# Performance work log

Hardware: AMD Instinct MI355X
Metric: run time of the kernel (lower is better)

## Reference

```python
import jax, jax.numpy as jnp
import numpy as np

BS, F, C, H, W = 2, 8, 64, 128, 128
HEADS = 4

def build_edges(bs, f):
    rows, cols, ec = [], [], 0
    for b in range(bs):
        s = b * (2 * f + 2)
        v = list(range(s, s + f)); d = list(range(s + f, s + 2 * f))
        t = s + 2 * f; g = t + 1
        for grp in (v, d, v + d, v + d, v + d + [t], [t], [g]):
            rows += grp; cols += [ec] * len(grp); ec += 1
    return np.asarray(rows, np.int32), np.asarray(cols, np.int32), ec

ROW, COL, NUM_EDGES = build_edges(BS, F)

def conv2d_s2(x, w, b):  # Conv2d k3 s2 p1 + ReLU
    y = jax.lax.conv_general_dilated(x, w, (2, 2), [(1, 1), (1, 1)],
        dimension_numbers=('NCHW', 'OIHW', 'NCHW'))
    return jax.nn.relu(y + b[None, :, None, None])

def conv_t2(x, w, b):  # ConvTranspose2d k3 s2 p1 op1 + ReLU; w: (in,out,3,3)
    wt = jnp.flip(w, (2, 3)).transpose(1, 0, 2, 3)
    y = jax.lax.conv_general_dilated(x, wt, (1, 1), [(1, 2), (1, 2)],
        lhs_dilation=(2, 2), dimension_numbers=('NCHW', 'OIHW', 'NCHW'))
    return jax.nn.relu(y + b[None, :, None, None])

def layer_norm(x, eps=1e-5):  # affine params are default ones/zeros
    mu = x.mean(-1, keepdims=True)
    var = ((x - mu) ** 2).mean(-1, keepdims=True)
    return (x - mu) / jnp.sqrt(var + eps)

def group_norm(x, groups=32, eps=1e-5):
    n, c = x.shape
    xg = x.reshape(n, groups, c // groups)
    mu = xg.mean(-1, keepdims=True)
    var = ((xg - mu) ** 2).mean(-1, keepdims=True)
    return ((xg - mu) / jnp.sqrt(var + eps)).reshape(n, c)

def se_layer(x, w1, w2):  # squeeze over node dim 0
    y = jax.nn.sigmoid(jax.nn.relu(x.mean(0) @ w1.T) @ w2.T)
    return x * y

def hypergraph_conv(x, lin_w, att, edge_w, edge_attr, out_ch):
    # PyG HypergraphConv, use_attention=True, attention_mode='node', heads=4,
    # concat=False, bias=False, eval mode (dropout inactive)
    n = x.shape[0]
    xl = (x @ lin_w.T).reshape(n, HEADS, out_ch)
    ea = (edge_attr @ lin_w.T).reshape(-1, HEADS, out_ch)
    a = (jnp.concatenate([xl[ROW], ea[COL]], axis=-1) * att).sum(-1)  # (E, heads)
    a = jax.nn.leaky_relu(a, 0.2)
    a = jnp.exp(a - jax.ops.segment_max(a, COL, num_segments=NUM_EDGES)[COL])
    a = a / (jax.ops.segment_sum(a, COL, num_segments=NUM_EDGES)[COL] + 1e-16)
    D = jax.ops.segment_sum(edge_w[COL], ROW, num_segments=n)
    D = jnp.where(D > 0, 1.0 / D, 0.0)
    B = jax.ops.segment_sum(jnp.ones(ROW.shape[0], x.dtype), COL, num_segments=NUM_EDGES)
    B = jnp.where(B > 0, 1.0 / B, 0.0)
    e = jax.ops.segment_sum(B[COL][:, None, None] * a[:, :, None] * xl[ROW], COL, num_segments=NUM_EDGES)
    o = jax.ops.segment_sum(D[ROW][:, None, None] * a[:, :, None] * e[COL], ROW, num_segments=n)
    return o.mean(1)  # concat=False -> head mean

def setup_inputs() -> dict:
    key = jax.random.key(0)
    ks = jax.random.split(key, 32)
    def n(k, shape, s=1.0):
        return jax.random.normal(k, shape, jnp.float32) * s
    def u(k, shape):
        return jax.random.uniform(k, shape, jnp.float32)
    return {
        'vision_feat': n(ks[0], (BS, F, C, H, W)), 'vision_pos': n(ks[1], (BS, F, C, H, W), 0.1),
        'motion_feat': n(ks[2], (BS, F, C, H, W)), 'motion_pos': n(ks[3], (BS, F, C, H, W), 0.1),
        'text_feat': n(ks[4], (BS, C, 16)), 'text_pos': n(ks[5], (BS, C, 16), 0.1),
        'cv1_w': n(ks[6], (2 * C, C, 3, 3), 0.04), 'cv1_b': n(ks[7], (2 * C,), 0.01),
        'cv2_w': n(ks[8], (4 * C, 2 * C, 3, 3), 0.03), 'cv2_b': n(ks[9], (4 * C,), 0.01),
        'dc1_w': n(ks[10], (2 * C, C, 3, 3), 0.04), 'dc1_b': n(ks[11], (2 * C,), 0.01),
        'dc2_w': n(ks[12], (4 * C, 2 * C, 3, 3), 0.03), 'dc2_b': n(ks[13], (4 * C,), 0.01),
        'tc1_w': n(ks[14], (4 * C, 2 * C, 3, 3), 0.03), 'tc1_b': n(ks[15], (2 * C,), 0.01),
        'tc2_w': n(ks[16], (2 * C, C, 3, 3), 0.04), 'tc2_b': n(ks[17], (C,), 0.01),
        'lin1_w': n(ks[18], (HEADS * 8 * C, 4 * C), 0.06), 'att1': n(ks[19], (1, HEADS, 16 * C), 0.05),
        'lin2_w': n(ks[20], (HEADS * 4 * C, 8 * C), 0.04), 'att2': n(ks[21], (1, HEADS, 8 * C), 0.05),
        'ew1': u(ks[22], (2 * F * BS + 2,)), 'ew2': u(ks[23], (2 * F * BS + 2,)),
        'ea1': u(ks[24], (2 * F * BS + 2, 4 * C)), 'ea2': u(ks[25], (2 * F * BS + 2, 8 * C)),
        'se1_w1': n(ks[26], (8 * C // 16, 8 * C), 0.06), 'se1_w2': n(ks[27], (8 * C, 8 * C // 16), 0.15),
        'se2_w1': n(ks[28], (4 * C // 16, 4 * C), 0.08), 'se2_w2': n(ks[29], (4 * C, 4 * C // 16), 0.2),
    }

def reference(vision_feat, vision_pos, motion_feat, motion_pos, text_feat, text_pos,
              cv1_w, cv1_b, cv2_w, cv2_b, dc1_w, dc1_b, dc2_w, dc2_b,
              tc1_w, tc1_b, tc2_w, tc2_b, lin1_w, att1, lin2_w, att2,
              ew1, ew2, ea1, ea2, se1_w1, se1_w2, se2_w1, se2_w2):
    bs, f, c, h, w = vision_feat.shape
    # text_pool: AdaptiveMaxPool1d(4) on L=16 -> exact windows of 4; view(bs,-1)
    tn = (text_feat + text_pos).reshape(bs, c, 4, 4).max(-1).reshape(bs, 4 * c)
    v0 = (vision_feat + vision_pos).reshape(bs * f, c, h, w)
    v1 = conv2d_s2(v0, cv1_w, cv1_b)          # (bs*f, 2c, h/2, w/2)
    v2 = conv2d_s2(v1, cv2_w, cv2_b)          # (bs*f, 4c, h/4, w/4)
    vn = layer_norm(v2.max((2, 3)))           # AdaptiveMaxPool2d(1) + LayerNorm
    d0 = (motion_feat + motion_pos).reshape(bs * f, c, h, w)
    dn = layer_norm(conv2d_s2(conv2d_s2(d0, dc1_w, dc1_b), dc2_w, dc2_b).max((2, 3)))
    vb = vn.reshape(bs, f, 4 * c); db = dn.reshape(bs, f, 4 * c)
    obs = tn + (vb + db).mean(1)              # observer = mean(text+v+d) over frames
    x = jnp.concatenate([vb, db, tn[:, None], obs[:, None]], axis=1).reshape(bs * (2 * f + 2), 4 * c)
    x = se_layer(group_norm(jax.nn.relu(hypergraph_conv(x, lin1_w, att1, ew1, ea1, 8 * c))), se1_w1, se1_w2)
    x = se_layer(group_norm(jax.nn.relu(hypergraph_conv(x, lin2_w, att2, ew2, ea2, 4 * c))), se2_w1, se2_w2)
    xb = x.reshape(bs, 2 * f + 2, 4 * c)
    # obs_pool: AdaptiveMaxPool1d(c) on L=4c -> windows of 4
    observers = (tn + xb[:, -1]).reshape(bs, c, 4).max(-1)
    vg = xb[:, :f].reshape(bs * f, 4 * c)
    # bilinear upsample of 1x1 == broadcast; transconv doubles size so the
    # subsequent F.interpolate calls to (h/2,w/2) and (h,w) are identities
    vr = v2 + vg[:, :, None, None]
    vr = v1 + conv_t2(vr, tc1_w, tc1_b)
    vr = v0 + conv_t2(vr, tc2_w, tc2_b)
    return vr, observers
```

## Files before the change

kernel.cpp:

```cpp
#include <hip/hip_runtime.h>
#include <hip/hip_bf16.h>
#include <cstddef>
#include <cstdint>

#define DEV_INLINE __device__ __forceinline__
#define AS1 __attribute__((address_space(1)))
#define AS3 __attribute__((address_space(3)))

typedef __attribute__((ext_vector_type(8))) short short8;
typedef __attribute__((ext_vector_type(4))) float f32x4;
typedef __attribute__((ext_vector_type(2))) float f32x2;
typedef __attribute__((ext_vector_type(4))) unsigned short us4;

DEV_INLINE unsigned short f2bf(float f) {
  uint32_t u = __builtin_bit_cast(uint32_t, f);
  uint32_t r = (u + 0x7fffu + ((u >> 16) & 1u)) >> 16;
  return (unsigned short)r;
}
DEV_INLINE float bf2f(unsigned short u) {
  return __builtin_bit_cast(float, (uint32_t)u << 16);
}

DEV_INLINE void gl_lds16(const float* g, float* l) {
  __builtin_amdgcn_global_load_lds((AS1 void*)const_cast<float*>(g),
                                   (AS3 void*)l, 16, 0, 0);
}

__device__ __constant__ int c_cs[15] = {0,8,16,32,48,65,66,67,75,83,99,115,132,133,134};
__device__ __constant__ int c_row[134] = {
  0,1,2,3,4,5,6,7,
  8,9,10,11,12,13,14,15,
  0,1,2,3,4,5,6,7,8,9,10,11,12,13,14,15,
  0,1,2,3,4,5,6,7,8,9,10,11,12,13,14,15,
  0,1,2,3,4,5,6,7,8,9,10,11,12,13,14,15,16,
  16,
  17,
  18,19,20,21,22,23,24,25,
  26,27,28,29,30,31,32,33,
  18,19,20,21,22,23,24,25,26,27,28,29,30,31,32,33,
  18,19,20,21,22,23,24,25,26,27,28,29,30,31,32,33,
  18,19,20,21,22,23,24,25,26,27,28,29,30,31,32,33,34,
  34,
  35
};
__device__ __constant__ int c_col[134] = {
  0,0,0,0,0,0,0,0,
  1,1,1,1,1,1,1,1,
  2,2,2,2,2,2,2,2,2,2,2,2,2,2,2,2,
  3,3,3,3,3,3,3,3,3,3,3,3,3,3,3,3,
  4,4,4,4,4,4,4,4,4,4,4,4,4,4,4,4,4,
  5,
  6,
  7,7,7,7,7,7,7,7,
  8,8,8,8,8,8,8,8,
  9,9,9,9,9,9,9,9,9,9,9,9,9,9,9,9,
  10,10,10,10,10,10,10,10,10,10,10,10,10,10,10,10,
  11,11,11,11,11,11,11,11,11,11,11,11,11,11,11,11,11,
  12,
  13
};

__global__ __launch_bounds__(512) void k_prep(const float* __restrict__ a,
                                              const float* __restrict__ b,
                                              unsigned short* __restrict__ o) {
  __shared__ float sbuf[32 * 260];
  int bid = blockIdx.x;
  int y = bid & 127, n = bid >> 7;
  int t = threadIdx.x;
  int w = t >> 6, lane = t & 63;
  int cio = lane >> 5;
  int xg4 = (lane & 31) * 4;
  const size_t base = ((size_t)n * 64) * 16384 + (size_t)y * 128;
#pragma unroll
  for (int k = 0; k < 4; ++k) {
    int c = w * 4 + k;
    gl_lds16(a + base + (size_t)(2 * c + cio) * 16384 + xg4, &sbuf[c * 260]);
  }
  __syncthreads();
  auto rd = [&](int ci, int x) {
    return sbuf[(ci >> 1) * 260 + (ci & 1) * 128 + x];
  };
  float av[2][8];
#pragma unroll
  for (int it = 0; it < 2; ++it) {
    int i = t + it * 512;
    int x = i >> 3, cq = i & 7;
#pragma unroll
    for (int j = 0; j < 8; ++j) av[it][j] = rd(cq * 8 + j, x);
  }
  __syncthreads();
#pragma unroll
  for (int k = 0; k < 4; ++k) {
    int c = w * 4 + k;
    gl_lds16(b + base + (size_t)(2 * c + cio) * 16384 + xg4, &sbuf[c * 260]);
  }
  __syncthreads();
  unsigned int* op = (unsigned int*)(o + (((size_t)n * 128 + y) * 128) * 64);
#pragma unroll
  for (int it = 0; it < 2; ++it) {
    int i = t + it * 512;
    int x = i >> 3, cq = i & 7;
    uint4 v;
    unsigned int vv[4];
#pragma unroll
    for (int jj = 0; jj < 4; ++jj) {
      unsigned int lo = f2bf(av[it][2 * jj]     + rd(cq * 8 + 2 * jj, x));
      unsigned int hi = f2bf(av[it][2 * jj + 1] + rd(cq * 8 + 2 * jj + 1, x));
      vv[jj] = lo | (hi << 16);
    }
    v.x = vv[0]; v.y = vv[1]; v.z = vv[2]; v.w = vv[3];
    *reinterpret_cast<uint4*>(op + x * 32 + cq * 4) = v;
  }
}

__global__ void k_wtrans_all(const float* __restrict__ cv1w, const float* __restrict__ dc1w,
                             const float* __restrict__ cv2w, const float* __restrict__ dc2w,
                             const float* __restrict__ tc1w, const float* __restrict__ tc2w,
                             unsigned short* __restrict__ wtb) {
  int idx = blockIdx.x * 256 + threadIdx.x;
  const float* src; int off, lci, lco; bool tra;
  if (idx < 73728)        { src = cv1w; off = 0;       lci = 6; lco = 7; tra = false; }
  else if (idx < 147456)  { src = dc1w; off = 73728;   lci = 6; lco = 7; tra = false; }
  else if (idx < 442368)  { src = cv2w; off = 147456;  lci = 7; lco = 8; tra = false; }
  else if (idx < 737280)  { src = dc2w; off = 442368;  lci = 7; lco = 8; tra = false; }
  else if (idx < 1032192) { src = tc1w; off = 737280;  lci = 8; lco = 7; tra = true;  }
  else if (idx < 1105920) { src = tc2w; off = 1032192; lci = 7; lco = 6; tra = true;  }
  else return;
  int l = idx - off;
  int ci = l & ((1 << lci) - 1);
  int r = l >> lci;
  int co = r & ((1 << lco) - 1);
  int tap = r >> lco;
  size_t si = tra ? (((size_t)ci << lco) + co) * 9 + tap
                  : (((size_t)co << lci) + ci) * 9 + tap;
  wtb[idx] = f2bf(src[si]);
}

template<int CI, int CO, int HO, int WO, int ROUT, bool SPLIT_IN>
__global__ __launch_bounds__(512, 3) void k_conv_mfma_b(
    const unsigned short* __restrict__ in0, const unsigned short* __restrict__ in1,
    const unsigned short* __restrict__ wT0, const unsigned short* __restrict__ wT1,
    const float* __restrict__ b0, const float* __restrict__ b1,
    unsigned short* __restrict__ outn) {
  constexpr int HIN = HO * 2, WIN = WO * 2;
  constexpr int XHP = WO + 2;
  constexpr int R = 2 * ROUT + 1;
  constexpr int NPOS = R * 2 * XHP;
  static_assert(NPOS <= 512, "one staging position per thread");
  constexpr int NCS = CI / 32;
  constexpr int CB = CO / 128;
  constexpr int OB = HO / ROUT;
  __shared__ short8 sIn[4 * NPOS];
  int bid = blockIdx.x;
  int cb = bid % CB; bid /= CB;
  int oyb = bid % OB; int n = bid / OB;
  int br = n >> 4;
  const unsigned short* in = SPLIT_IN ? (br ? in1 : in0) : in0;
  const unsigned short* wT = br ? wT1 : wT0;
  const float* bias = br ? b1 : b0;
  int ni = SPLIT_IN ? (n & 15) : n;
  int tid = threadIdx.x;
  int wid = tid >> 6, lane = tid & 63;
  int wm = wid >> 1, wn = wid & 1;
  int llo = lane & 15, lhi = lane >> 4;
  f32x4 acc[2][2] = {};
  const int iy0 = oyb * (2 * ROUT) - 1;
  bool sact = tid < NPOS;
  int sx = 0, siy = 0; bool sok = false;
  if (sact) {
    int xh = tid % XHP; int q2 = tid / XHP;
    int par = q2 & 1, l = q2 >> 1;
    sx = 2 * xh + par - 1;
    siy = iy0 + l;
    sok = (sx >= 0 && sx < WIN && siy >= 0 && siy < HIN);
    if (!sok) { sx = 0; siy = 0; }
  }
  short8 rv[4];
  auto loadr = [&](int cs) {
    if (sact) {
      const unsigned short* gp = in + ((((size_t)ni * HIN + siy) * WIN + sx) * CI + cs * 32);
#pragma unroll
      for (int c = 0; c < 4; ++c) {
        short8 v = {};
        if (sok) v = *reinterpret_cast<const short8*>(gp + c * 8);
        rv[c] = v;
      }
    }
  };
  auto writes = [&]() {
    if (sact) {
#pragma unroll
      for (int c = 0; c < 4; ++c) sIn[c * NPOS + tid] = rv[c];
    }
  };
  loadr(0);
  for (int cs = 0; cs < NCS; ++cs) {
    writes();
    __syncthreads();
    if (cs + 1 < NCS) loadr(cs + 1);
    short8 afr9[9][2];
#pragma unroll
    for (int tap = 0; tap < 9; ++tap)
#pragma unroll
      for (int m = 0; m < 2; ++m) {
        int co = cb * 128 + wm * 32 + m * 16 + llo;
        afr9[tap][m] = *reinterpret_cast<const short8*>(wT + (((size_t)tap * CO + co) * CI + cs * 32 + lhi * 8));
      }
#pragma unroll
    for (int tap = 0; tap < 9; ++tap) {
      const int ky = tap / 3, kx = tap % 3;
      short8 bfr[2];
#pragma unroll
      for (int n2 = 0; n2 < 2; ++n2) {
        int pix = wn * 32 + n2 * 16 + llo;
        int oyl = (ROUT == 2) ? (pix >> 5) : 0;
        int ox = pix - oyl * WO;
        int lrow = 2 * oyl + ky;
        int pos = (lrow * 2 + (kx & 1)) * XHP + ox + (kx >> 1);
        bfr[n2] = sIn[lhi * NPOS + pos];
      }
#pragma unroll
      for (int m = 0; m < 2; ++m)
#pragma unroll
        for (int n2 = 0; n2 < 2; ++n2)
          acc[m][n2] = __builtin_amdgcn_mfma_f32_16x16x32_bf16(afr9[tap][m], bfr[n2], acc[m][n2], 0, 0, 0);
    }
    __syncthreads();
  }
#pragma unroll
  for (int m = 0; m < 2; ++m) {
    int co0 = cb * 128 + wm * 32 + m * 16 + lhi * 4;
    f32x4 bv = *reinterpret_cast<const f32x4*>(bias + co0);
#pragma unroll
    for (int n2 = 0; n2 < 2; ++n2) {
      int pix = wn * 32 + n2 * 16 + llo;
      int oyl = (ROUT == 2) ? (pix >> 5) : 0;
      int ox = pix - oyl * WO;
      int oy = oyb * ROUT + oyl;
      us4 pk;
      pk[0] = f2bf(fmaxf(acc[m][n2][0] + bv[0], 0.f));
      pk[1] = f2bf(fmaxf(acc[m][n2][1] + bv[1], 0.f));
      pk[2] = f2bf(fmaxf(acc[m][n2][2] + bv[2], 0.f));
      pk[3] = f2bf(fmaxf(acc[m][n2][3] + bv[3], 0.f));
      *reinterpret_cast<us4*>(outn + ((((size_t)n * HO + oy) * WO + ox) * CO + co0)) = pk;
    }
  }
}

template<int CI, int CO, int Hi, int Wi, int QR, bool OBF, bool GADD>
__global__ __launch_bounds__(256, 3) void k_deconv_mfma(
    const unsigned short* __restrict__ in,
    const unsigned short* __restrict__ wT,
    const float* __restrict__ bias,
    const unsigned short* __restrict__ resn,
    const float* __restrict__ gsrc,
    unsigned short* __restrict__ outn,
    float* __restrict__ outc) {
  constexpr int QC = 64 / QR;
  constexpr int WP = Wi + 1;
  constexpr int NPOS = (QR + 1) * WP;
  static_assert(NPOS <= 256, "one staging position per thread");
  constexpr int NCS = CI / 32;
  constexpr int CB = CO / 64;
  constexpr int OB = Hi / QR;
  constexpr int Ho = Hi * 2, Wo = Wi * 2;
  __shared__ short8 sIn[4 * NPOS];
  int bid = blockIdx.x;
  int cb = bid % CB; bid /= CB;
  int oyb = bid % OB; int n = bid / OB;
  int tid = threadIdx.x;
  int wid = tid >> 6, lane = tid & 63;
  int wm = wid >> 1, wn = wid & 1;
  int llo = lane & 15, lhi = lane >> 4;
  int qy0 = oyb * QR;
  const float* g = nullptr;
  if constexpr (GADD) g = gsrc + ((size_t)((n >> 3) * 18 + (n & 7))) * 256;
  f32x4 acc[4][2][2] = {};
  constexpr int tap_p[9] = {3,2,3,1,0,1,3,2,3};
  constexpr int tap_b[9] = {3,2,2,1,0,0,1,0,0};
  bool sact = tid < NPOS;
  int sx = 0, siy = 0; bool sok = false;
  if (sact) {
    sx = tid % WP;
    siy = qy0 + tid / WP;
    sok = (sx < Wi && siy < Hi);
    if (!sok) { sx = 0; siy = 0; }
  }
  short8 rv[4];
  auto loadr = [&](int cs) {
    if (sact) {
      const unsigned short* gp = in + (((size_t)(n * Hi + siy) * Wi + sx) * CI + cs * 32);
#pragma unroll
      for (int c = 0; c < 4; ++c) {
        short8 v = {};
        if (sok) {
          v = *reinterpret_cast<const short8*>(gp + c * 8);
          if constexpr (GADD) {
#pragma unroll
            for (int j = 0; j < 8; ++j) {
              float fv = bf2f((unsigned short)v[j]) + g[cs * 32 + c * 8 + j];
              v[j] = (short)f2bf(fv);
            }
          }
        }
        rv[c] = v;
      }
    }
  };
  auto writes = [&]() {
    if (sact) {
#pragma unroll
      for (int c = 0; c < 4; ++c) sIn[c * NPOS + tid] = rv[c];
    }
  };
  loadr(0);
  for (int cs = 0; cs < NCS; ++cs) {
    writes();
    __syncthreads();
    if (cs + 1 < NCS) loadr(cs + 1);
    short8 bfr[2][4];
#pragma unroll
    for (int n2 = 0; n2 < 2; ++n2) {
      int pix = wn * 32 + n2 * 16 + llo;
      int qyl = pix / QC, qx = pix % QC;
#pragma unroll
      for (int bs = 0; bs < 4; ++bs) {
        int pos = (qyl + (bs >> 1)) * WP + qx + (bs & 1);
        bfr[n2][bs] = sIn[lhi * NPOS + pos];
      }
    }
#pragma unroll
    for (int m = 0; m < 2; ++m) {
      short8 afr9[9];
#pragma unroll
      for (int tap = 0; tap < 9; ++tap) {
        int co = cb * 64 + wm * 32 + m * 16 + llo;
        afr9[tap] = *reinterpret_cast<const short8*>(wT + (((size_t)tap * CO + co) * CI + cs * 32 + lhi * 8));
      }
#pragma unroll
      for (int tap = 0; tap < 9; ++tap)
#pragma unroll
        for (int n2 = 0; n2 < 2; ++n2)
          acc[tap_p[tap]][m][n2] = __builtin_amdgcn_mfma_f32_16x16x32_bf16(
              afr9[tap], bfr[n2][tap_b[tap]], acc[tap_p[tap]][m][n2], 0, 0, 0);
    }
    __syncthreads();
  }
#pragma unroll
  for (int m = 0; m < 2; ++m) {
    int co0 = cb * 64 + wm * 32 + m * 16 + lhi * 4;
    f32x4 bv = *reinterpret_cast<const f32x4*>(bias + co0);
#pragma unroll
    for (int n2 = 0; n2 < 2; ++n2) {
      int pix = wn * 32 + n2 * 16 + llo;
      int qyl = pix / QC, qx = pix % QC;
      int qy = qy0 + qyl;
      if constexpr (OBF) {
#pragma unroll
        for (int p = 0; p < 4; ++p) {
          int oy = 2 * qy + (p >> 1);
          int ox = 2 * qx + (p & 1);
          size_t ad = ((size_t)(n * Ho + oy) * Wo + ox) * CO + co0;
          us4 r = *reinterpret_cast<const us4*>(resn + ad);
          us4 pk;
#pragma unroll
          for (int c = 0; c < 4; ++c)
            pk[c] = f2bf(bf2f(r[c]) + fmaxf(acc[p][m][n2][c] + bv[c], 0.f));
          *reinterpret_cast<us4*>(outn + ad) = pk;
        }
      } else {
        int qx2 = 2 * qx;
#pragma unroll
        for (int dy = 0; dy < 2; ++dy) {
          int oy = 2 * qy + dy;
          size_t rb = ((size_t)(n * Ho + oy) * Wo + qx2) * CO + co0;
          us4 r0 = *reinterpret_cast<const us4*>(resn + rb);
          us4 r1 = *reinterpret_cast<const us4*>(resn + rb + CO);
#pragma unroll
          for (int c = 0; c < 4; ++c) {
            f32x2 st;
            st[0] = bf2f(r0[c]) + fmaxf(acc[dy * 2][m][n2][c] + bv[c], 0.f);
            st[1] = bf2f(r1[c]) + fmaxf(acc[dy * 2 + 1][m][n2][c] + bv[c], 0.f);
            __builtin_nontemporal_store(st,
                reinterpret_cast<f32x2*>(outc + ((size_t)(n * CO + co0 + c) * Ho + oy) * Wo + qx2));
          }
        }
      }
    }
  }
}

__global__ __launch_bounds__(256) void k_max_part(const unsigned short* __restrict__ x,
                                                  float* __restrict__ pmax) {
  int n = blockIdx.x >> 3, pg = blockIdx.x & 7;
  int t = threadIdx.x;
  int c8 = t & 31;
  int ps = t >> 5;
  const unsigned short* base = x + (size_t)n * 262144 + (size_t)pg * 32768 + (size_t)c8 * 8;
  float m[8];
#pragma unroll
  for (int j = 0; j < 8; ++j) m[j] = -1e30f;
  for (int p = ps * 16; p < ps * 16 + 16; ++p) {
    short8 v = *reinterpret_cast<const short8*>(base + (size_t)p * 256);
#pragma unroll
    for (int j = 0; j < 8; ++j) m[j] = fmaxf(m[j], bf2f((unsigned short)v[j]));
  }
  __shared__ float sred[8][264];
#pragma unroll
  for (int j = 0; j < 8; ++j) sred[ps][c8 * 8 + j] = m[j];
  __syncthreads();
  float mm = sred[0][t];
#pragma unroll
  for (int g = 1; g < 8; ++g) mm = fmaxf(mm, sred[g][t]);
  pmax[((size_t)n * 8 + pg) * 256 + t] = mm;
}

__global__ __launch_bounds__(256) void k_ln(const float* __restrict__ pmax,
                                            float* __restrict__ out) {
  int n = blockIdx.x, ch = threadIdx.x;
  float m = -1e30f;
#pragma unroll
  for (int g = 0; g < 8; ++g)
    m = fmaxf(m, pmax[((size_t)n * 8 + g) * 256 + ch]);
  __shared__ float r1[256], r2[256];
  r1[ch] = m; __syncthreads();
  for (int s = 128; s > 0; s >>= 1) { if (ch < s) r1[ch] += r1[ch + s]; __syncthreads(); }
  float mu = r1[0] * (1.f / 256.f);
  float d = m - mu;
  r2[ch] = d * d; __syncthreads();
  for (int s = 128; s > 0; s >>= 1) { if (ch < s) r2[ch] += r2[ch + s]; __syncthreads(); }
  out[(size_t)n * 256 + ch] = d * rsqrtf(r2[0] * (1.f / 256.f) + 1e-5f);
}

__global__ void k_build_x(const float* __restrict__ tf, const float* __restrict__ tp,
                          const float* __restrict__ nb,
                          float* __restrict__ tn, float* __restrict__ x0) {
  int b = blockIdx.x, ch = threadIdx.x;
  int c4 = ch >> 2, j = ch & 3;
  const float* p = tf + ((size_t)b * 64 + c4) * 16 + j * 4;
  const float* q = tp + ((size_t)b * 64 + c4) * 16 + j * 4;
  float tv = p[0] + q[0];
  tv = fmaxf(tv, p[1] + q[1]);
  tv = fmaxf(tv, p[2] + q[2]);
  tv = fmaxf(tv, p[3] + q[3]);
  tn[(size_t)b * 256 + ch] = tv;
  const float* dn = nb;
  const float* vn = nb + 16 * 256;
  float s = 0.f;
  for (int f = 0; f < 8; ++f) {
    float vv = vn[((size_t)b * 8 + f) * 256 + ch];
    float dd = dn[((size_t)b * 8 + f) * 256 + ch];
    s += vv + dd;
    x0[((size_t)b * 18 + f) * 256 + ch] = vv;
    x0[((size_t)b * 18 + 8 + f) * 256 + ch] = dd;
  }
  x0[((size_t)b * 18 + 16) * 256 + ch] = tv;
  x0[((size_t)b * 18 + 17) * 256 + ch] = tv + s * (1.f / 8.f);
}

__global__ __launch_bounds__(256) void k_gnn_lin(
    const float* __restrict__ x, const float* __restrict__ ea,
    const float* __restrict__ w, float* __restrict__ y, int K, int M) {
  int chunks = M >> 8;
  int r = blockIdx.x / chunks;
  int ob = (blockIdx.x % chunks) * 256 + threadIdx.x;
  const float* src = (r < 36) ? (x + (size_t)r * K) : (ea + (size_t)(r - 36) * K);
  __shared__ __align__(16) float sxr[512];
  for (int k = threadIdx.x; k < K; k += 256) sxr[k] = src[k];
  __syncthreads();
  const float4* w4 = reinterpret_cast<const float4*>(w + (size_t)ob * K);
  const float4* x4 = reinterpret_cast<const float4*>(sxr);
  float acc = 0.f;
  int k4 = K >> 2;
  for (int k = 0; k < k4; ++k) {
    float4 a = x4[k], b = w4[k];
    acc += a.x * b.x + a.y * b.y + a.z * b.z + a.w * b.w;
  }
  y[(size_t)r * M + ob] = acc;
}

template<int OC>
__global__ __launch_bounds__(256) void k_gnn_attsm(
    const float* __restrict__ y, const float* __restrict__ att,
    float* __restrict__ attw) {
  int t = threadIdx.x;
  __shared__ float sx_s[144], seb_s[60];
  __shared__ float a_s[536];
  if (t < 200) {
    int r = t >> 2, h = t & 3;
    const float4* row = reinterpret_cast<const float4*>(y + ((size_t)r * 4 + h) * OC);
    const float4* ar = reinterpret_cast<const float4*>(att + (size_t)h * 2 * OC + (r < 36 ? 0 : OC));
    float s = 0.f;
#pragma unroll 4
    for (int k = 0; k < OC / 4; ++k) {
      float4 a = row[k], b = ar[k];
      s += a.x * b.x + a.y * b.y + a.z * b.z + a.w * b.w;
    }
    if (r < 36) sx_s[r * 4 + h] = s; else seb_s[(r - 36) * 4 + h] = s;
  }
  __syncthreads();
  for (int idx = t; idx < 536; idx += 256) {
    int i = idx >> 2, h = idx & 3;
    float v = sx_s[c_row[i] * 4 + h] + seb_s[c_col[i] * 4 + h];
    a_s[idx] = (v > 0.f) ? v : 0.2f * v;
  }
  __syncthreads();
  if (t < 56) {
    int c = t >> 2, h = t & 3;
    int st = c_cs[c], en = c_cs[c + 1];
    float m = -1e30f;
    for (int i = st; i < en; ++i) m = fmaxf(m, a_s[i * 4 + h]);
    float s = 0.f;
    for (int i = st; i < en; ++i) { float e = __expf(a_s[i * 4 + h] - m); a_s[i * 4 + h] = e; s += e; }
    float inv = 1.f / (s + 1e-16f);
    for (int i = st; i < en; ++i) a_s[i * 4 + h] *= inv;
  }
  __syncthreads();
  for (int idx = t; idx < 536; idx += 256) attw[idx] = a_s[idx];
}

template<int OC>
__global__ __launch_bounds__(256) void k_edge_agg(
    const float* __restrict__ y, const float* __restrict__ attw,
    float* __restrict__ eb) {
  int idx = blockIdx.x * 256 + threadIdx.x;
  if (idx >= 14 * 4 * OC) return;
  int ch = idx % OC;
  int h = (idx / OC) & 3;
  int c = idx / (4 * OC);
  int st = c_cs[c], en = c_cs[c + 1];
  float s = 0.f;
  for (int i = st; i < en; ++i)
    s += attw[i * 4 + h] * y[(size_t)c_row[i] * (4 * OC) + h * OC + ch];
  eb[idx] = s * (1.f / (float)(en - st));
}

template<int OC>
__global__ __launch_bounds__(256) void k_node_agg(
    const float* __restrict__ attw, const float* __restrict__ eb,
    const float* __restrict__ ew, float* __restrict__ ho) {
  int idx = blockIdx.x * 256 + threadIdx.x;
  if (idx >= 36 * OC) return;
  int ch = idx % OC;
  int node = idx / OC;
  int b = node / 18, ln = node % 18;
  int ncols, cols[4], gis[4];
  if (ln < 16) {
    ncols = 4;
    cols[0] = b * 7 + (ln < 8 ? 0 : 1); gis[0] = b * 67 + ln;
    cols[1] = b * 7 + 2; gis[1] = b * 67 + 16 + ln;
    cols[2] = b * 7 + 3; gis[2] = b * 67 + 32 + ln;
    cols[3] = b * 7 + 4; gis[3] = b * 67 + 48 + ln;
  } else if (ln == 16) {
    ncols = 2;
    cols[0] = b * 7 + 4; gis[0] = b * 67 + 64;
    cols[1] = b * 7 + 5; gis[1] = b * 67 + 65;
    cols[2] = cols[3] = 0; gis[2] = gis[3] = 0;
  } else {
    ncols = 1;
    cols[0] = b * 7 + 6; gis[0] = b * 67 + 66;
    cols[1] = cols[2] = cols[3] = 0; gis[1] = gis[2] = gis[3] = 0;
  }
  float dsum = 0.f;
#pragma unroll
  for (int k = 0; k < 4; ++k) if (k < ncols) dsum += ew[cols[k]];
  float D = dsum > 0.f ? 1.f / dsum : 0.f;
  float s = 0.f;
#pragma unroll
  for (int k = 0; k < 4; ++k) {
    if (k < ncols) {
#pragma unroll
      for (int h = 0; h < 4; ++h)
        s += attw[gis[k] * 4 + h] * eb[((size_t)cols[k] * 4 + h) * OC + ch];
    }
  }
  ho[idx] = fmaxf(0.25f * D * s, 0.f);
}

template<int C, int Cr>
__global__ __launch_bounds__(512) void k_gn_se(
    const float* __restrict__ hin, const float* __restrict__ w1,
    const float* __restrict__ w2, float* __restrict__ x) {
  int t = threadIdx.x;
  constexpr int gs = C >> 5;
  for (int idx = t; idx < 36 * 32; idx += 512) {
    int node = idx >> 5, g = idx & 31;
    const float* p = hin + (size_t)node * C + g * gs;
    float s = 0.f, s2 = 0.f;
#pragma unroll
    for (int k = 0; k < gs; ++k) { float v = p[k]; s += v; s2 += v * v; }
    float mu = s * (1.f / gs);
    float var = s2 * (1.f / gs) - mu * mu;
    float inv = rsqrtf(fmaxf(var, 0.f) + 1e-5f);
    float* q = x + (size_t)node * C + g * gs;
#pragma unroll
    for (int k = 0; k < gs; ++k) q[k] = (p[k] - mu) * inv;
  }
  __threadfence_block();
  __syncthreads();
  __shared__ float smean[C];
  __shared__ float spart[Cr][17];
  __shared__ float shid[Cr];
  __shared__ float sscale[C];
  if (t < C) {
    float s = 0.f;
    for (int nn = 0; nn < 36; ++nn) s += x[(size_t)nn * C + t];
    smean[t] = s * (1.f / 36.f);
  }
  __syncthreads();
  if (t < Cr * 16) {
    int hid = t >> 4, sub = t & 15;
    constexpr int CH = C / 16;
    float s = 0.f;
#pragma unroll
    for (int k = 0; k < CH; ++k)
      s += w1[(size_t)hid * C + sub * CH + k] * smean[sub * CH + k];
    spart[hid][sub] = s;
  }
  __syncthreads();
  if (t < Cr) {
    float s = 0.f;
#pragma unroll
    for (int k = 0; k < 16; ++k) s += spart[t][k];
    shid[t] = fmaxf(s, 0.f);
  }
  __syncthreads();
  if (t < C) {
    float s = 0.f;
#pragma unroll
    for (int k = 0; k < Cr; ++k) s += w2[(size_t)t * Cr + k] * shid[k];
    sscale[t] = 1.f / (1.f + __expf(-s));
  }
  __syncthreads();
  for (int idx = t; idx < 36 * C; idx += 512) x[idx] *= sscale[idx % C];
}

__global__ void k_obs(const float* __restrict__ tn, const float* __restrict__ x2,
                      float* __restrict__ out) {
  int t = threadIdx.x;
  if (t >= 128) return;
  int b = t >> 6, ch = t & 63;
  const float* a = tn + (size_t)b * 256 + ch * 4;
  const float* c = x2 + ((size_t)b * 18 + 17) * 256 + ch * 4;
  float m = a[0] + c[0];
  m = fmaxf(m, a[1] + c[1]);
  m = fmaxf(m, a[2] + c[2]);
  m = fmaxf(m, a[3] + c[3]);
  out[b * 64 + ch] = m;
}

extern "C" void kernel_launch(void* const* d_in, const int* in_sizes, int n_in,
                              void* d_out, int out_size, void* d_ws, size_t ws_size,
                              hipStream_t stream) {
  (void)in_sizes; (void)n_in; (void)out_size; (void)ws_size;
  const float* vf    = (const float*)d_in[0];
  const float* vp    = (const float*)d_in[1];
  const float* mf    = (const float*)d_in[2];
  const float* mp    = (const float*)d_in[3];
  const float* tf    = (const float*)d_in[4];
  const float* tp    = (const float*)d_in[5];
  const float* cv1w  = (const float*)d_in[6];
  const float* cv1b  = (const float*)d_in[7];
  const float* cv2w  = (const float*)d_in[8];
  const float* cv2b  = (const float*)d_in[9];
  const float* dc1w  = (const float*)d_in[10];
  const float* dc1b  = (const float*)d_in[11];
  const float* dc2w  = (const float*)d_in[12];
  const float* dc2b  = (const float*)d_in[13];
  const float* tc1w  = (const float*)d_in[14];
  const float* tc1b  = (const float*)d_in[15];
  const float* tc2w  = (const float*)d_in[16];
  const float* tc2b  = (const float*)d_in[17];
  const float* lin1w = (const float*)d_in[18];
  const float* att1  = (const float*)d_in[19];
  const float* lin2w = (const float*)d_in[20];
  const float* att2  = (const float*)d_in[21];
  const float* ew1   = (const float*)d_in[22];
  const float* ew2   = (const float*)d_in[23];
  const float* ea1   = (const float*)d_in[24];
  const float* ea2   = (const float*)d_in[25];
  const float* se1w1 = (const float*)d_in[26];
  const float* se1w2 = (const float*)d_in[27];
  const float* se2w1 = (const float*)d_in[28];
  const float* se2w2 = (const float*)d_in[29];

  float* ws  = (float*)d_ws;
  float* out = (float*)d_out;

  unsigned short* p0nm = (unsigned short*)(ws);
  unsigned short* p0nv = (unsigned short*)(ws + 8388608);
  unsigned short* q1nb = (unsigned short*)(ws + 16777216);
  unsigned short* wtb  = (unsigned short*)(ws + 25165824);
  float* sm   = ws + 25718784;
  float* tn   = sm;
  float* nb   = sm + 512;
  float* x0   = sm + 8704;
  float* xl   = sm + 17920;
  float* eb   = sm + 120520;
  float* ho   = sm + 149192;
  float* x1   = sm + 167624;
  float* x2   = sm + 186056;
  float* attw = sm + 195272;
  float* pmax = sm + 195904;

  unsigned short* v2nb = (unsigned short*)d_out;
  unsigned short* t1n = (unsigned short*)(ws);

  unsigned short* wTc1 = wtb;
  unsigned short* wTd1 = wtb + 73728;
  unsigned short* wTc2 = wtb + 147456;
  unsigned short* wTd2 = wtb + 442368;
  unsigned short* wTt1 = wtb + 737280;
  unsigned short* wTt2 = wtb + 1032192;

  k_wtrans_all<<<4320, 256, 0, stream>>>(cv1w, dc1w, cv2w, dc2w, tc1w, tc2w, wtb);

  k_prep<<<2048, 512, 0, stream>>>(mf, mp, p0nm);
  k_prep<<<2048, 512, 0, stream>>>(vf, vp, p0nv);

  k_conv_mfma_b<64, 128, 64, 64, 1, true><<<2048, 512, 0, stream>>>(
      p0nm, p0nv, wTd1, wTc1, dc1b, cv1b, q1nb);
  k_conv_mfma_b<128, 256, 32, 32, 2, false><<<1024, 512, 0, stream>>>(
      q1nb, nullptr, wTd2, wTc2, dc2b, cv2b, v2nb);
  k_max_part<<<256, 256, 0, stream>>>(v2nb, pmax);
  k_ln<<<32, 256, 0, stream>>>(pmax, nb);

  k_build_x<<<2, 256, 0, stream>>>(tf, tp, nb, tn, x0);

  k_gnn_lin<<<50 * 8, 256, 0, stream>>>(x0, ea1, lin1w, xl, 256, 2048);
  k_gnn_attsm<512><<<1, 256, 0, stream>>>(xl, att1, attw);
  k_edge_agg<512><<<112, 256, 0, stream>>>(xl, attw, eb);
  k_node_agg<512><<<72, 256, 0, stream>>>(attw, eb, ew1, ho);
  k_gn_se<512, 32><<<1, 512, 0, stream>>>(ho, se1w1, se1w2, x1);

  k_gnn_lin<<<50 * 4, 256, 0, stream>>>(x1, ea2, lin2w, xl, 512, 1024);
  k_gnn_attsm<256><<<1, 256, 0, stream>>>(xl, att2, attw);
  k_edge_agg<256><<<56, 256, 0, stream>>>(xl, attw, eb);
  k_node_agg<256><<<36, 256, 0, stream>>>(attw, eb, ew2, ho);
  k_gn_se<256, 16><<<1, 512, 0, stream>>>(ho, se2w1, se2w2, x2);

  k_obs<<<1, 128, 0, stream>>>(tn, x2, out + 16777216);

  unsigned short* v2nv = v2nb + 4194304;
  unsigned short* q1nv = q1nb + 8388608;
  k_deconv_mfma<256, 128, 32, 32, 2, true, true><<<512, 256, 0, stream>>>(
      v2nv, wTt1, tc1b, q1nv, x2, t1n, nullptr);
  k_deconv_mfma<128, 64, 64, 64, 1, false, false><<<1024, 256, 0, stream>>>(
      t1n, wTt2, tc2b, p0nv, nullptr, nullptr, out);
}
```

Baseline: 485.0 us.

## Stage larger input channel slabs in LDS for conv and deconv MFMA kernels

Result: no change. 488.4 us (+0.7%).

```diff
diff --git a/kernel.cpp b/kernel.cpp
--- a/kernel.cpp
+++ b/kernel.cpp
@@ -21,8 +21,8 @@
   return __builtin_bit_cast(float, (uint32_t)u << 16);
 }
 
-DEV_INLINE void gl_lds16(const float* g, float* l) {
-  __builtin_amdgcn_global_load_lds((AS1 void*)const_cast<float*>(g),
+DEV_INLINE void gl_lds16(const void* g, void* l) {
+  __builtin_amdgcn_global_load_lds((AS1 void*)const_cast<void*>(g),
                                    (AS3 void*)l, 16, 0, 0);
 }
 
@@ -147,10 +147,10 @@
   constexpr int R = 2 * ROUT + 1;
   constexpr int NPOS = R * 2 * XHP;
   static_assert(NPOS <= 512, "one staging position per thread");
-  constexpr int NCS = CI / 32;
+  constexpr int NST = CI / 64;
   constexpr int CB = CO / 128;
   constexpr int OB = HO / ROUT;
-  __shared__ short8 sIn[4 * NPOS];
+  __shared__ short8 sIn[8 * NPOS];
   int bid = blockIdx.x;
   int cb = bid % CB; bid /= CB;
   int oyb = bid % OB; int n = bid / OB;
@@ -175,57 +175,55 @@
     sok = (sx >= 0 && sx < WIN && siy >= 0 && siy < HIN);
     if (!sok) { sx = 0; siy = 0; }
   }
-  short8 rv[4];
-  auto loadr = [&](int cs) {
+  auto stage = [&](int st) {
     if (sact) {
-      const unsigned short* gp = in + ((((size_t)ni * HIN + siy) * WIN + sx) * CI + cs * 32);
-#pragma unroll
-      for (int c = 0; c < 4; ++c) {
+      const unsigned short* gp = in + ((((size_t)ni * HIN + siy) * WIN + sx) * CI + st * 64);
+      short8 rv[8];
+#pragma unroll
+      for (int c = 0; c < 8; ++c) {
         short8 v = {};
         if (sok) v = *reinterpret_cast<const short8*>(gp + c * 8);
         rv[c] = v;
       }
+#pragma unroll
+      for (int c = 0; c < 8; ++c) sIn[c * NPOS + tid] = rv[c];
     }
   };
-  auto writes = [&]() {
-    if (sact) {
-#pragma unroll
-      for (int c = 0; c < 4; ++c) sIn[c * NPOS + tid] = rv[c];
-    }
-  };
-  loadr(0);
-  for (int cs = 0; cs < NCS; ++cs) {
-    writes();
+  for (int st = 0; st < NST; ++st) {
+    if (st > 0) __syncthreads();
+    stage(st);
     __syncthreads();
-    if (cs + 1 < NCS) loadr(cs + 1);
-    short8 afr9[9][2];
-#pragma unroll
-    for (int tap = 0; tap < 9; ++tap)
-#pragma unroll
-      for (int m = 0; m < 2; ++m) {
-        int co = cb * 128 + wm * 32 + m * 16 + llo;
-        afr9[tap][m] = *reinterpret_cast<const short8*>(wT + (((size_t)tap * CO + co) * CI + cs * 32 + lhi * 8));
+#pragma unroll
+    for (int sub = 0; sub < 2; ++sub) {
+      int cs = st * 2 + sub;
+      short8 afr9[9][2];
+#pragma unroll
+      for (int tap = 0; tap < 9; ++tap)
+#pragma unroll
+        for (int m = 0; m < 2; ++m) {
+          int co = cb * 128 + wm * 32 + m * 16 + llo;
+          afr9[tap][m] = *reinterpret_cast<const short8*>(wT + (((size_t)tap * CO + co) * CI + cs * 32 + lhi * 8));
+        }
+#pragma unroll
+      for (int tap = 0; tap < 9; ++tap) {
+        const int ky = tap / 3, kx = tap % 3;
+        short8 bfr[2];
+#pragma unroll
+        for (int n2 = 0; n2 < 2; ++n2) {
+          int pix = wn * 32 + n2 * 16 + llo;
+          int oyl = (ROUT == 2) ? (pix >> 5) : 0;
+          int ox = pix - oyl * WO;
+          int lrow = 2 * oyl + ky;
+          int pos = (lrow * 2 + (kx & 1)) * XHP + ox + (kx >> 1);
+          bfr[n2] = sIn[(sub * 4 + lhi) * NPOS + pos];
+        }
+#pragma unroll
+        for (int m = 0; m < 2; ++m)
+#pragma unroll
+          for (int n2 = 0; n2 < 2; ++n2)
+            acc[m][n2] = __builtin_amdgcn_mfma_f32_16x16x32_bf16(afr9[tap][m], bfr[n2], acc[m][n2], 0, 0, 0);
       }
-#pragma unroll
-    for (int tap = 0; tap < 9; ++tap) {
-      const int ky = tap / 3, kx = tap % 3;
-      short8 bfr[2];
-#pragma unroll
-      for (int n2 = 0; n2 < 2; ++n2) {
-        int pix = wn * 32 + n2 * 16 + llo;
-        int oyl = (ROUT == 2) ? (pix >> 5) : 0;
-        int ox = pix - oyl * WO;
-        int lrow = 2 * oyl + ky;
-        int pos = (lrow * 2 + (kx & 1)) * XHP + ox + (kx >> 1);
-        bfr[n2] = sIn[lhi * NPOS + pos];
-      }
-#pragma unroll
-      for (int m = 0; m < 2; ++m)
-#pragma unroll
-        for (int n2 = 0; n2 < 2; ++n2)
-          acc[m][n2] = __builtin_amdgcn_mfma_f32_16x16x32_bf16(afr9[tap][m], bfr[n2], acc[m][n2], 0, 0, 0);
-    }
-    __syncthreads();
+    }
   }
 #pragma unroll
   for (int m = 0; m < 2; ++m) {
@@ -260,11 +258,12 @@
   constexpr int WP = Wi + 1;
   constexpr int NPOS = (QR + 1) * WP;
   static_assert(NPOS <= 256, "one staging position per thread");
+  constexpr int NCHK = CI / 8;
   constexpr int NCS = CI / 32;
   constexpr int CB = CO / 64;
   constexpr int OB = Hi / QR;
   constexpr int Ho = Hi * 2, Wo = Wi * 2;
-  __shared__ short8 sIn[4 * NPOS];
+  __shared__ short8 sIn[NCHK * NPOS];
   int bid = blockIdx.x;
   int cb = bid % CB; bid /= CB;
   int oyb = bid % OB; int n = bid / OB;
@@ -278,55 +277,42 @@
   f32x4 acc[4][2][2] = {};
   constexpr int tap_p[9] = {3,2,3,1,0,1,3,2,3};
   constexpr int tap_b[9] = {3,2,2,1,0,0,1,0,0};
-  bool sact = tid < NPOS;
-  int sx = 0, siy = 0; bool sok = false;
-  if (sact) {
-    sx = tid % WP;
-    siy = qy0 + tid / WP;
-    sok = (sx < Wi && siy < Hi);
-    if (!sok) { sx = 0; siy = 0; }
-  }
-  short8 rv[4];
-  auto loadr = [&](int cs) {
+  {
+    bool sact = tid < NPOS;
     if (sact) {
-      const unsigned short* gp = in + (((size_t)(n * Hi + siy) * Wi + sx) * CI + cs * 32);
-#pragma unroll
-      for (int c = 0; c < 4; ++c) {
+      int sx = tid % WP;
+      int siy = qy0 + tid / WP;
+      bool sok = (sx < Wi && siy < Hi);
+      const unsigned short* gp = in + (((size_t)(n * Hi + (sok ? siy : 0)) * Wi + (sok ? sx : 0)) * CI);
+#pragma unroll
+      for (int c = 0; c < NCHK; ++c) {
         short8 v = {};
         if (sok) {
           v = *reinterpret_cast<const short8*>(gp + c * 8);
           if constexpr (GADD) {
 #pragma unroll
             for (int j = 0; j < 8; ++j) {
-              float fv = bf2f((unsigned short)v[j]) + g[cs * 32 + c * 8 + j];
+              float fv = bf2f((unsigned short)v[j]) + g[c * 8 + j];
               v[j] = (short)f2bf(fv);
             }
           }
         }
-        rv[c] = v;
+        sIn[c * NPOS + tid] = v;
       }
     }
-  };
-  auto writes = [&]() {
-    if (sact) {
-#pragma unroll
-      for (int c = 0; c < 4; ++c) sIn[c * NPOS + tid] = rv[c];
-    }
-  };
-  loadr(0);
+  }
+  __syncthreads();
+  int pix = wn * 32;
   for (int cs = 0; cs < NCS; ++cs) {
-    writes();
-    __syncthreads();
-    if (cs + 1 < NCS) loadr(cs + 1);
     short8 bfr[2][4];
 #pragma unroll
     for (int n2 = 0; n2 < 2; ++n2) {
-      int pix = wn * 32 + n2 * 16 + llo;
-      int qyl = pix / QC, qx = pix % QC;
+      int px = wn * 32 + n2 * 16 + llo;
+      int qyl = px / QC, qx = px % QC;
 #pragma unroll
       for (int bs = 0; bs < 4; ++bs) {
         int pos = (qyl + (bs >> 1)) * WP + qx + (bs & 1);
-        bfr[n2][bs] = sIn[lhi * NPOS + pos];
+        bfr[n2][bs] = sIn[(cs * 4 + lhi) * NPOS + pos];
       }
     }
 #pragma unroll
@@ -344,16 +330,16 @@
           acc[tap_p[tap]][m][n2] = __builtin_amdgcn_mfma_f32_16x16x32_bf16(
               afr9[tap], bfr[n2][tap_b[tap]], acc[tap_p[tap]][m][n2], 0, 0, 0);
     }
-    __syncthreads();
-  }
+  }
+  (void)pix;
 #pragma unroll
   for (int m = 0; m < 2; ++m) {
     int co0 = cb * 64 + wm * 32 + m * 16 + lhi * 4;
     f32x4 bv = *reinterpret_cast<const f32x4*>(bias + co0);
 #pragma unroll
     for (int n2 = 0; n2 < 2; ++n2) {
-      int pix = wn * 32 + n2 * 16 + llo;
-      int qyl = pix / QC, qx = pix % QC;
+      int px = wn * 32 + n2 * 16 + llo;
+      int qyl = px / QC, qx = px % QC;
       int qy = qy0 + qyl;
       if constexpr (OBF) {
 #pragma unroll
```
